# Kernel optimization log

Measured on AMD Instinct MI355X. Metric: run time of the kernel, lower is better.

Reference implementation:

```python
import jax, jax.numpy as jnp
import numpy as np

N, E, D, DE, DIN, L = 50000, 500000, 128, 16, 64, 4
EPS = 1e-5


def setup_inputs() -> dict:
    key = jax.random.key(0)
    ks = jax.random.split(key, 32)
    inp = {
        "x": jax.random.normal(ks[0], (N, DIN), dtype=jnp.float32),
        "edge_index": jax.random.randint(ks[1], (2, E), 0, N, dtype=jnp.int32),
        "edge_attr": jax.random.normal(ks[2], (E, DE), dtype=jnp.float32),
        "Win": jax.random.normal(ks[3], (DIN, D), dtype=jnp.float32) * 0.05,
        "b_in": jnp.zeros((D,), dtype=jnp.float32),
    }
    i = 4
    def lin(shape):
        nonlocal i
        w = jax.random.normal(ks[i], shape, dtype=jnp.float32) * 0.05
        i += 1
        return w
    def bn_params():
        nonlocal i
        g = jnp.ones((L, D), dtype=jnp.float32)
        b = jnp.zeros((L, D), dtype=jnp.float32)
        m = jax.random.normal(ks[i], (L, D), dtype=jnp.float32) * 0.1
        v = jax.random.uniform(ks[i + 1], (L, D), dtype=jnp.float32, minval=0.5, maxval=1.5)
        i += 2
        return g, b, m, v
    # message MLP: Linear(2D+DE -> D), BN, ReLU, Drop(eval), Linear(D -> D), BN, ReLU
    inp["Wm1"] = lin((L, 2 * D + DE, D)); inp["bm1"] = jnp.zeros((L, D), jnp.float32)
    inp["gm1"], inp["bem1"], inp["mm1"], inp["vm1"] = bn_params()
    inp["Wm2"] = lin((L, D, D)); inp["bm2"] = jnp.zeros((L, D), jnp.float32)
    inp["gm2"], inp["bem2"], inp["mm2"], inp["vm2"] = bn_params()
    # update MLP: Linear(2D -> D), BN, ReLU, Drop(eval), Linear(D -> D), BN, ReLU
    inp["Wu1"] = lin((L, 2 * D, D)); inp["bu1"] = jnp.zeros((L, D), jnp.float32)
    inp["gu1"], inp["beu1"], inp["mu1"], inp["vu1"] = bn_params()
    inp["Wu2"] = lin((L, D, D)); inp["bu2"] = jnp.zeros((L, D), jnp.float32)
    inp["gu2"], inp["beu2"], inp["mu2"], inp["vu2"] = bn_params()
    return inp


def _bn(x, g, b, m, v):
    # BatchNorm1d in eval mode: normalize with running stats
    return (x - m) * jax.lax.rsqrt(v + EPS) * g + b


def reference(x, edge_index, edge_attr, Win, b_in,
              Wm1, bm1, gm1, bem1, mm1, vm1,
              Wm2, bm2, gm2, bem2, mm2, vm2,
              Wu1, bu1, gu1, beu1, mu1, vu1,
              Wu2, bu2, gu2, beu2, mu2, vu2):
    h = x @ Win + b_in                       # (n, d)
    src, dst = edge_index[0], edge_index[1]  # PyG: row0 = source j, row1 = target i
    n = h.shape[0]
    num_layers = Wm1.shape[0]
    for l in range(num_layers):
        # message: concat(h_i, h_j, edge_attr) -> MLP psi
        m = jnp.concatenate([h[dst], h[src], edge_attr], axis=-1)   # (e, 2d+de)
        m = jax.nn.relu(_bn(m @ Wm1[l] + bm1[l], gm1[l], bem1[l], mm1[l], vm1[l]))
        m = jax.nn.relu(_bn(m @ Wm2[l] + bm2[l], gm2[l], bem2[l], mm2[l], vm2[l]))
        # aggregate: scatter-add messages to target nodes
        agg = jax.ops.segment_sum(m, dst, num_segments=n)           # (n, d)
        # update: concat(h, agg) -> MLP phi
        u = jnp.concatenate([h, agg], axis=-1)                      # (n, 2d)
        u = jax.nn.relu(_bn(u @ Wu1[l] + bu1[l], gu1[l], beu1[l], mu1[l], vu1[l]))
        u = jax.nn.relu(_bn(u @ Wu2[l] + bu2[l], gu2[l], beu2[l], mu2[l], vu2[l]))
        h = h + u                                                   # residual
    return h
```

## Files before the change

kernel.cpp:

```cpp
#include <hip/hip_runtime.h>
#include <hip/hip_fp16.h>

#define D 128
#define DE 16
#define NL 4
#define EPSV 1e-5f
#define S_U1 8
#define S_U2 4
#define NBMSG 512
#define MSG_LDS 75776

using f32x4  = __attribute__((ext_vector_type(4))) float;
using bf16x8 = __attribute__((ext_vector_type(8))) short;
typedef _Float16 f16x8 __attribute__((ext_vector_type(8)));

#define MFMAB(a, b, c) __builtin_amdgcn_mfma_f32_16x16x32_bf16((a), (b), (c), 0, 0, 0)
#define MFMAH(a, b, c) __builtin_amdgcn_mfma_f32_16x16x32_f16((a), (b), (c), 0, 0, 0)

union H8 { int4 i; unsigned int u[4]; f16x8 f; };

__device__ __forceinline__ unsigned short f2bf(float x) {
  unsigned int u = __float_as_uint(x);
  u = (u + 0x7FFFu + ((u >> 16) & 1u)) >> 16;
  return (unsigned short)u;
}

__device__ __forceinline__ unsigned short f2h(float x) {
  return __half_as_ushort(__float2half(x));
}

__device__ __forceinline__ float h2f(unsigned short x) {
  return __half2float(__ushort_as_half(x));
}

__device__ __forceinline__ unsigned int pk_add(unsigned int a, unsigned int b) {
  unsigned int r;
  asm("v_pk_add_f16 %0, %1, %2" : "=v"(r) : "v"(a), "v"(b));
  return r;
}
__device__ __forceinline__ unsigned int pk_relu(unsigned int a) {
  unsigned int r;
  asm("v_pk_max_f16 %0, %1, 0" : "=v"(r) : "v"(a));
  return r;
}

__device__ __forceinline__ void gload_lds16(const void* gp, void* lp) {
  typedef __attribute__((address_space(1))) unsigned int as1_u32;
  typedef __attribute__((address_space(3))) unsigned int as3_u32;
  __builtin_amdgcn_global_load_lds((as1_u32*)(unsigned long long)gp,
                                   (as3_u32*)(unsigned int)(unsigned long long)lp,
                                   16, 0, 0);
}

__device__ __forceinline__ bf16x8 pack8(float4 a, float4 b) {
  bf16x8 o;
  o[0] = (short)f2bf(a.x); o[1] = (short)f2bf(a.y);
  o[2] = (short)f2bf(a.z); o[3] = (short)f2bf(a.w);
  o[4] = (short)f2bf(b.x); o[5] = (short)f2bf(b.y);
  o[6] = (short)f2bf(b.z); o[7] = (short)f2bf(b.w);
  return o;
}

__device__ __forceinline__ int4 pack8h(float4 a, float4 b) {
  int4 o;
  o.x = (int)((unsigned)f2h(a.x) | ((unsigned)f2h(a.y) << 16));
  o.y = (int)((unsigned)f2h(a.z) | ((unsigned)f2h(a.w) << 16));
  o.z = (int)((unsigned)f2h(b.x) | ((unsigned)f2h(b.y) << 16));
  o.w = (int)((unsigned)f2h(b.z) | ((unsigned)f2h(b.w) << 16));
  return o;
}

__global__ void wprep_kernel(const float* __restrict__ W, const float* __restrict__ g,
                             const float* __restrict__ v, unsigned short* __restrict__ out,
                             int K, int S, int total) {
  int idx = blockIdx.x * 256 + threadIdx.x;
  if (idx >= total) return;
  int e = idx & 7, l0 = (idx >> 3) & 63, f = idx >> 9;
  int n = f & 7, sf = f >> 3, s = sf % S, l = sf / S;
  int k = s * 32 + ((l0 >> 4) << 3) + e;
  int c = (n << 4) + (l0 & 15);
  float val = 0.f;
  if (k < K) {
    float sc = g[l * D + c] * rsqrtf(v[l * D + c] + EPSV);
    val = W[((size_t)(l * K + k)) * D + c] * sc;
  }
  out[idx] = f2bf(val);
}

__global__ void wprep16_kernel(const float* __restrict__ W, const float* __restrict__ g,
                               const float* __restrict__ v, unsigned short* __restrict__ out,
                               int Ktot, int ko, int Kact, int S, int total) {
  int idx = blockIdx.x * 256 + threadIdx.x;
  if (idx >= total) return;
  int e = idx & 7, l0 = (idx >> 3) & 63, f = idx >> 9;
  int n = f & 7, sf = f >> 3, s = sf % S, l = sf / S;
  int k = s * 32 + ((l0 >> 4) << 3) + e;
  int c = (n << 4) + (l0 & 15);
  float val = 0.f;
  if (k < Kact) {
    float sc = g[l * D + c] * rsqrtf(v[l * D + c] + EPSV);
    val = W[((size_t)(l * Ktot + ko + k)) * D + c] * sc;
  }
  out[idx] = f2h(val);
}

__global__ void wprepz_kernel(const float* __restrict__ W1, const float* __restrict__ g,
                              const float* __restrict__ v, unsigned short* __restrict__ out,
                              int total) {
  int idx = blockIdx.x * 256 + threadIdx.x;
  if (idx >= total) return;
  int e = idx & 7, l0 = (idx >> 3) & 63, f = idx >> 9;
  int n = f & 15, sf = f >> 4, s = sf & 3, l = sf >> 2;
  int k = s * 32 + ((l0 >> 4) << 3) + e;
  int c = ((n & 7) << 4) + (l0 & 15);
  int row = (n < 8) ? k : 128 + k;
  float sc = g[l * D + c] * rsqrtf(v[l * D + c] + EPSV);
  float val = W1[((size_t)(l * 272 + row)) * D + c] * sc;
  out[idx] = f2bf(val);
}

__global__ void wprepx_kernel(const float* __restrict__ Win, unsigned short* __restrict__ out) {
  int idx = blockIdx.x * 256 + threadIdx.x;
  if (idx >= 8192) return;
  int e = idx & 7, l0 = (idx >> 3) & 63, f = idx >> 9;
  int n = f & 7, s = f >> 3;
  int k = s * 32 + ((l0 >> 4) << 3) + e;
  int c = (n << 4) + (l0 & 15);
  out[idx] = f2bf(Win[k * D + c]);
}

__global__ void cvtx_kernel(const float* __restrict__ x, unsigned short* __restrict__ xbf, int n8) {
  int idx = blockIdx.x * 256 + threadIdx.x;
  if (idx >= n8) return;
  float4 a = reinterpret_cast<const float4*>(x)[idx * 2];
  float4 b = reinterpret_cast<const float4*>(x)[idx * 2 + 1];
  reinterpret_cast<bf16x8*>(xbf)[idx] = pack8(a, b);
}

__global__ void bprep_kernel(const float* __restrict__ b, const float* __restrict__ g,
                             const float* __restrict__ be, const float* __restrict__ m,
                             const float* __restrict__ v, float* __restrict__ out) {
  int idx = blockIdx.x * 256 + threadIdx.x;
  if (idx >= NL * D) return;
  float s = g[idx] * rsqrtf(v[idx] + EPSV);
  out[idx] = (b[idx] - m[idx]) * s + be[idx];
}

__global__ __launch_bounds__(256)
void xz_kernel(const unsigned short* __restrict__ xbf,
               const unsigned short* __restrict__ Wxf,
               const float* __restrict__ bin,
               const unsigned short* __restrict__ Wzf,
               const float* __restrict__ b1,
               float* __restrict__ h,
               unsigned short* __restrict__ hbf,
               unsigned short* __restrict__ zds, int N) {
  __shared__ unsigned short m1ls[4][16 * 128];
  const int tid = threadIdx.x, wid = tid >> 6, lane = tid & 63, g = lane >> 4, r = lane & 15;
  const int nbase = blockIdx.x * 64;
  const int nr = nbase + wid * 16 + r;
  const int ar = (nr < N) ? nr : (N - 1);

  bf16x8 aX[2];
#pragma unroll
  for (int s = 0; s < 2; ++s)
    aX[s] = *reinterpret_cast<const bf16x8*>(xbf + (size_t)ar * 64 + s * 32 + g * 8);

  f32x4 acc[8];
#pragma unroll
  for (int n = 0; n < 8; ++n)
#pragma unroll
    for (int q = 0; q < 4; ++q) acc[n][q] = 0.f;
#pragma unroll
  for (int s = 0; s < 2; ++s)
#pragma unroll
    for (int n = 0; n < 8; ++n)
      acc[n] = MFMAB(aX[s], *reinterpret_cast<const bf16x8*>(Wxf + (((s * 8 + n) << 9) + (lane << 3))), acc[n]);

  float bia[8];
#pragma unroll
  for (int n = 0; n < 8; ++n) bia[n] = bin[n * 16 + r];

  unsigned short* m1w = &m1ls[wid][0];
#pragma unroll
  for (int j = 0; j < 4; ++j) {
    int node = nbase + wid * 16 + g * 4 + j;
    if (node < N) {
#pragma unroll
      for (int n = 0; n < 8; ++n) {
        int col = n * 16 + r;
        float hv = acc[n][j] + bia[n];
        h[(size_t)node * D + col] = hv;
        unsigned short hb = f2bf(hv);
        hbf[(size_t)node * D + col] = hb;
        int row0 = g * 4 + j;
        m1w[row0 * 128 + (col ^ ((row0 & 7) << 3))] = hb;
      }
    }
  }

  bf16x8 aZ[4];
#pragma unroll
  for (int s = 0; s < 4; ++s) {
    int k0 = s * 32 + g * 8;
    aZ[s] = *reinterpret_cast<const bf16x8*>(m1w + r * 128 + (k0 ^ ((r & 7) << 3)));
  }
  float bz[8];
#pragma unroll
  for (int n = 0; n < 8; ++n) bz[n] = b1[n * 16 + r];
#pragma unroll
  for (int half = 0; half < 2; ++half) {
    f32x4 zacc[8];
#pragma unroll
    for (int n = 0; n < 8; ++n)
#pragma unroll
      for (int q = 0; q < 4; ++q) zacc[n][q] = 0.f;
#pragma unroll
    for (int s = 0; s < 4; ++s)
#pragma unroll
      for (int n = 0; n < 8; ++n)
        zacc[n] = MFMAB(aZ[s], *reinterpret_cast<const bf16x8*>(Wzf + (((s * 16 + half * 8 + n) << 9) + (lane << 3))), zacc[n]);
#pragma unroll
    for (int n = 0; n < 8; ++n)
#pragma unroll
      for (int j = 0; j < 4; ++j) {
        int node = nbase + wid * 16 + g * 4 + j;
        if (node < N) {
          float v = zacc[n][j] + (half == 0 ? bz[n] : 0.f);
          zds[(size_t)node * 256 + (half * 8 + n) * 16 + r] = f2h(v);
        }
      }
  }
}

__global__ void hist_kernel(const int* __restrict__ eidx, int* __restrict__ hist, int E) {
  int e = blockIdx.x * 256 + threadIdx.x;
  if (e < E) atomicAdd(&hist[eidx[E + e]], 1);
}

__global__ void scan1_kernel(const int* __restrict__ hist, int* __restrict__ bsum, int N) {
  __shared__ int sb[256];
  int i = blockIdx.x * 256 + threadIdx.x;
  sb[threadIdx.x] = (i < N) ? hist[i] : 0;
  __syncthreads();
  for (int d = 128; d > 0; d >>= 1) {
    if (threadIdx.x < d) sb[threadIdx.x] += sb[threadIdx.x + d];
    __syncthreads();
  }
  if (threadIdx.x == 0) bsum[blockIdx.x] = sb[0];
}

__global__ void scan2_kernel(int* __restrict__ bsum, int nb) {
  __shared__ int sb[2][256];
  int t = threadIdx.x;
  int v = (t < nb) ? bsum[t] : 0;
  int p = 0;
  sb[0][t] = v; __syncthreads();
#pragma unroll
  for (int d = 1; d < 256; d <<= 1) {
    int nv = sb[p][t] + ((t >= d) ? sb[p][t - d] : 0);
    sb[p ^ 1][t] = nv; p ^= 1;
    __syncthreads();
  }
  if (t < nb) bsum[t] = sb[p][t] - v;
}

__global__ void scan3_kernel(int* __restrict__ hist, const int* __restrict__ bsum, int N) {
  __shared__ int sb[2][256];
  int i = blockIdx.x * 256 + threadIdx.x, t = threadIdx.x;
  int v = (i < N) ? hist[i] : 0;
  int p = 0;
  sb[0][t] = v; __syncthreads();
#pragma unroll
  for (int d = 1; d < 256; d <<= 1) {
    int nv = sb[p][t] + ((t >= d) ? sb[p][t - d] : 0);
    sb[p ^ 1][t] = nv; p ^= 1;
    __syncthreads();
  }
  if (i < N) hist[i] = sb[p][t] - v + bsum[blockIdx.x];
}

__global__ void scatter_kernel(const int* __restrict__ eidx, int* __restrict__ cursor,
                               int* __restrict__ dstS, int* __restrict__ srcS,
                               int* __restrict__ eidS, int E) {
  int e = blockIdx.x * 256 + threadIdx.x;
  if (e >= E) return;
  int d = eidx[E + e];
  int pos = atomicAdd(&cursor[d], 1);
  dstS[pos] = d;
  srcS[pos] = eidx[e];
  eidS[pos] = e;
}

__global__ void eperm_kernel(const float* __restrict__ eattr, const int* __restrict__ eidS,
                             unsigned short* __restrict__ ebfS, int E) {
  int i = blockIdx.x * 256 + threadIdx.x;
  if (i >= E) return;
  const float4* src = reinterpret_cast<const float4*>(eattr + (size_t)eidS[i] * DE);
  *reinterpret_cast<int4*>(ebfS + (size_t)i * DE) = pack8h(src[0], src[1]);
  *reinterpret_cast<int4*>(ebfS + (size_t)i * DE + 8) = pack8h(src[2], src[3]);
}

__global__ __launch_bounds__(512, 4)
void msg_kernel(const unsigned short* __restrict__ zds,
                const unsigned short* __restrict__ ebfS,
                const int* __restrict__ dstS,
                const int* __restrict__ srcS,
                const unsigned short* __restrict__ Wef,
                const unsigned short* __restrict__ W2f,
                const float* __restrict__ b2,
                unsigned short* __restrict__ msgb, int E, int T) {
  extern __shared__ char smem[];
  unsigned short* Wels = (unsigned short*)smem;
  unsigned short* W2ls = (unsigned short*)(smem + 8192);
  const int tid = threadIdx.x;
  const int wid = tid >> 6, lane = tid & 63, g = lane >> 4, r = lane & 15;
  unsigned short* zeb = (unsigned short*)(smem + 40960 + wid * 4352);

  gload_lds16(Wef + ((size_t)tid << 3), smem + (tid << 4));
#pragma unroll
  for (int i = 0; i < 4; ++i) {
    int idx = i * 512 + tid;
    gload_lds16(W2f + ((size_t)idx << 3), smem + 8192 + (idx << 4));
  }

  float bia2[8];
#pragma unroll
  for (int n = 0; n < 8; ++n) bia2[n] = b2[n * 16 + r];

  const int t0 = (int)(((long long)blockIdx.x * T) / gridDim.x);
  const int t1 = (int)(((long long)(blockIdx.x + 1) * T) / gridDim.x);

  __syncthreads();

  for (int t = t0; t < t1; ++t) {
    const int p0 = t * 128 + wid * 16 + r;
    const int ii0 = min(p0, E - 1);
    const int dst0 = dstS[ii0], src0 = srcS[ii0];

    H8 zd[4], zs[4];
#pragma unroll
    for (int s = 0; s < 4; ++s) {
      zd[s].i = *reinterpret_cast<const int4*>(zds + (size_t)dst0 * 256 + s * 32 + g * 8);
      zs[s].i = *reinterpret_cast<const int4*>(zds + (size_t)src0 * 256 + 128 + s * 32 + g * 8);
    }

    H8 aE;
    aE.i = make_int4(0, 0, 0, 0);
    if (g < 2) aE.i = *reinterpret_cast<const int4*>(ebfS + (size_t)ii0 * DE + g * 8);
    f32x4 ze[8];
#pragma unroll
    for (int n = 0; n < 8; ++n)
#pragma unroll
      for (int q = 0; q < 4; ++q) ze[n][q] = 0.f;
#pragma unroll
    for (int n = 0; n < 8; ++n) {
      f16x8 b = *reinterpret_cast<const f16x8*>(Wels + (n << 9) + (lane << 3));
      ze[n] = MFMAH(aE.f, b, ze[n]);
    }

#pragma unroll
    for (int n = 0; n < 8; ++n)
#pragma unroll
      for (int j = 0; j < 4; ++j) {
        int row = g * 4 + j;
        zeb[row * 136 + ((n * 2 + (r >> 3)) << 3) + (r & 7)] = f2h(ze[n][j]);
      }

    f32x4 c[8];
#pragma unroll
    for (int n = 0; n < 8; ++n)
#pragma unroll
      for (int q = 0; q < 4; ++q) c[n][q] = 0.f;

#pragma unroll
    for (int s = 0; s < 4; ++s) {
      H8 zeA, m;
      zeA.i = *reinterpret_cast<const int4*>(zeb + r * 136 + ((s * 4 + g) << 3));
#pragma unroll
      for (int w = 0; w < 4; ++w)
        m.u[w] = pk_relu(pk_add(pk_add(zd[s].u[w], zs[s].u[w]), zeA.u[w]));
      __builtin_amdgcn_s_setprio(1);
#pragma unroll
      for (int n = 0; n < 8; ++n) {
        f16x8 b = *reinterpret_cast<const f16x8*>(W2ls + ((s * 8 + n) << 9) + (lane << 3));
        c[n] = MFMAH(m.f, b, c[n]);
      }
      __builtin_amdgcn_s_setprio(0);
    }

#pragma unroll
    for (int n = 0; n < 8; ++n) {
      unsigned int lo = (unsigned)f2h(fmaxf(c[n][0] + bia2[n], 0.f))
                      | ((unsigned)f2h(fmaxf(c[n][1] + bia2[n], 0.f)) << 16);
      unsigned int hi = (unsigned)f2h(fmaxf(c[n][2] + bia2[n], 0.f))
                      | ((unsigned)f2h(fmaxf(c[n][3] + bia2[n], 0.f)) << 16);
      size_t addr8 = ((((size_t)t * 32 + wid * 4 + g) * 8 + n) * 16) + r;
      uint2 pk; pk.x = lo; pk.y = hi;
      *reinterpret_cast<uint2*>(msgb + addr8 * 4) = pk;
    }
  }
}

__global__ __launch_bounds__(256)
void reduce_kernel(const unsigned short* __restrict__ msgb,
                   const int* __restrict__ csr_end,
                   unsigned short* __restrict__ aggbf, int N) {
  const int tid = threadIdx.x, wid = tid >> 6, lane = tid & 63;
  const int er = lane >> 4, cg = lane & 15;
  for (int v = blockIdx.x * 4 + wid; v < N; v += gridDim.x * 4) {
    const int s = (v == 0) ? 0 : csr_end[v - 1];
    const int e = csr_end[v];
    float a[8];
#pragma unroll
    for (int n = 0; n < 8; ++n) a[n] = 0.f;
    const int qe = (e + 3) >> 2;
    for (int qb = (s >> 2); qb < qe; qb += 4) {
      int q = qb + er;
      if (q < qe) {
        size_t base8 = (size_t)q * 128 + cg;
        int p0 = 4 * q;
#pragma unroll
        for (int n = 0; n < 8; ++n) {
          uint2 d = *reinterpret_cast<const uint2*>(msgb + (base8 + (size_t)n * 16) * 4);
          float v0 = h2f((unsigned short)(d.x & 0xffff));
          float v1 = h2f((unsigned short)(d.x >> 16));
          float v2 = h2f((unsigned short)(d.y & 0xffff));
          float v3 = h2f((unsigned short)(d.y >> 16));
          a[n] += ((p0 >= s && p0 < e) ? v0 : 0.f)
                + ((p0 + 1 >= s && p0 + 1 < e) ? v1 : 0.f)
                + ((p0 + 2 >= s && p0 + 2 < e) ? v2 : 0.f)
                + ((p0 + 3 >= s && p0 + 3 < e) ? v3 : 0.f);
        }
      }
    }
#pragma unroll
    for (int n = 0; n < 8; ++n) {
      a[n] += __shfl_xor(a[n], 16);
      a[n] += __shfl_xor(a[n], 32);
    }
    if (er == 0) {
#pragma unroll
      for (int n = 0; n < 8; ++n)
        aggbf[(size_t)v * 128 + n * 16 + cg] = f2bf(a[n]);
    }
  }
}

__global__ __launch_bounds__(256, 3)
void node_kernel(const unsigned short* __restrict__ hbf,
                 const unsigned short* __restrict__ aggbf,
                 const unsigned short* __restrict__ W1f,
                 const unsigned short* __restrict__ W2f,
                 const float* __restrict__ b1,
                 const float* __restrict__ b2,
                 float* __restrict__ h,
                 unsigned short* __restrict__ hbfo,
                 const unsigned short* __restrict__ Wzf,
                 const float* __restrict__ b1n,
                 unsigned short* __restrict__ zds, int N) {
  __shared__ unsigned short m1ls[4][16 * 128];

  const int tid = threadIdx.x, wid = tid >> 6, lane = tid & 63, g = lane >> 4, r = lane & 15;
  const int nbase = blockIdx.x * 64;
  const int nr0 = nbase + wid * 16 + r;
  const int ar0 = (nr0 < N) ? nr0 : (N - 1);

  bf16x8 aH0[4], aG0[4];
#pragma unroll
  for (int s = 0; s < 4; ++s) {
    aH0[s] = *reinterpret_cast<const bf16x8*>(hbf + (size_t)ar0 * D + s * 32 + g * 8);
    aG0[s] = *reinterpret_cast<const bf16x8*>(aggbf + (size_t)ar0 * D + s * 32 + g * 8);
  }

  float hv[4][8];
#pragma unroll
  for (int j = 0; j < 4; ++j) {
    int node = nbase + wid * 16 + g * 4 + j;
    int an = (node < N) ? node : (N - 1);
#pragma unroll
    for (int n = 0; n < 8; ++n)
      hv[j][n] = h[(size_t)an * D + n * 16 + r];
  }

  float bia1[8], bia2[8];
#pragma unroll
  for (int n = 0; n < 8; ++n) { bia1[n] = b1[n * 16 + r]; bia2[n] = b2[n * 16 + r]; }

  f32x4 acc0[8];
#pragma unroll
  for (int n = 0; n < 8; ++n)
#pragma unroll
    for (int q = 0; q < 4; ++q) acc0[n][q] = 0.f;

#pragma unroll
  for (int s = 0; s < S_U1; ++s) {
    bf16x8 a0 = (s < 4) ? aH0[s & 3] : aG0[(s - 4) & 3];
#pragma unroll
    for (int n = 0; n < 8; ++n) {
      bf16x8 b = *reinterpret_cast<const bf16x8*>(W1f + (((s * 8 + n) << 9) + (lane << 3)));
      acc0[n] = MFMAB(a0, b, acc0[n]);
    }
  }

  unsigned short* m1w = &m1ls[wid][0];
#pragma unroll
  for (int n = 0; n < 8; ++n)
#pragma unroll
    for (int j = 0; j < 4; ++j) {
      int col = n * 16 + r;
      int row0 = g * 4 + j;
      m1w[row0 * 128 + (col ^ ((row0 & 7) << 3))] = f2bf(fmaxf(acc0[n][j] + bia1[n], 0.f));
    }

  f32x4 c0[8];
#pragma unroll
  for (int n = 0; n < 8; ++n)
#pragma unroll
    for (int q = 0; q < 4; ++q) c0[n][q] = 0.f;

#pragma unroll
  for (int s = 0; s < S_U2; ++s) {
    int k0 = s * 32 + g * 8;
    bf16x8 a0 = *reinterpret_cast<const bf16x8*>(m1w + r * 128 + (k0 ^ ((r & 7) << 3)));
#pragma unroll
    for (int n = 0; n < 8; ++n) {
      bf16x8 b = *reinterpret_cast<const bf16x8*>(W2f + (((s * 8 + n) << 9) + (lane << 3)));
      c0[n] = MFMAB(a0, b, c0[n]);
    }
  }

#pragma unroll
  for (int j = 0; j < 4; ++j) {
    int node = nbase + wid * 16 + g * 4 + j;
    if (node < N) {
#pragma unroll
      for (int n = 0; n < 8; ++n) {
        int col = n * 16 + r;
        float hvnew = hv[j][n] + fmaxf(c0[n][j] + bia2[n], 0.f);
        h[(size_t)node * D + col] = hvnew;
        unsigned short hb = f2bf(hvnew);
        hbfo[(size_t)node * D + col] = hb;
        int row0 = g * 4 + j;
        m1w[row0 * 128 + (col ^ ((row0 & 7) << 3))] = hb;
      }
    }
  }

  if (Wzf != nullptr) {
    bf16x8 aZ[4];
#pragma unroll
    for (int s = 0; s < 4; ++s) {
      int k0 = s * 32 + g * 8;
      aZ[s] = *reinterpret_cast<const bf16x8*>(m1w + r * 128 + (k0 ^ ((r & 7) << 3)));
    }
    float bz[8];
#pragma unroll
    for (int n = 0; n < 8; ++n) bz[n] = b1n[n * 16 + r];
#pragma unroll
    for (int half = 0; half < 2; ++half) {
      f32x4 zacc[8];
#pragma unroll
      for (int n = 0; n < 8; ++n)
#pragma unroll
        for (int q = 0; q < 4; ++q) zacc[n][q] = 0.f;
#pragma unroll
      for (int s = 0; s < 4; ++s)
#pragma unroll
        for (int n = 0; n < 8; ++n)
          zacc[n] = MFMAB(aZ[s], *reinterpret_cast<const bf16x8*>(Wzf + (((s * 16 + half * 8 + n) << 9) + (lane << 3))), zacc[n]);
#pragma unroll
      for (int n = 0; n < 8; ++n)
#pragma unroll
        for (int j = 0; j < 4; ++j) {
          int node = nbase + wid * 16 + g * 4 + j;
          if (node < N) {
            float v = zacc[n][j] + (half == 0 ? bz[n] : 0.f);
            zds[(size_t)node * 256 + (half * 8 + n) * 16 + r] = f2h(v);
          }
        }
    }
  }
}

extern "C" void kernel_launch(void* const* d_in, const int* in_sizes, int n_in,
                              void* d_out, int out_size, void* d_ws, size_t ws_size,
                              hipStream_t stream) {
  const float* x     = (const float*)d_in[0];
  const int*   eidx  = (const int*)d_in[1];
  const float* eattr = (const float*)d_in[2];
  const float* Win   = (const float*)d_in[3];
  const float* bin   = (const float*)d_in[4];
  const float* Wm1 = (const float*)d_in[5];  const float* bm1 = (const float*)d_in[6];
  const float* gm1 = (const float*)d_in[7];  const float* bem1 = (const float*)d_in[8];
  const float* mm1 = (const float*)d_in[9];  const float* vm1 = (const float*)d_in[10];
  const float* Wm2 = (const float*)d_in[11]; const float* bm2 = (const float*)d_in[12];
  const float* gm2 = (const float*)d_in[13]; const float* bem2 = (const float*)d_in[14];
  const float* mm2 = (const float*)d_in[15]; const float* vm2 = (const float*)d_in[16];
  const float* Wu1 = (const float*)d_in[17]; const float* bu1 = (const float*)d_in[18];
  const float* gu1 = (const float*)d_in[19]; const float* beu1 = (const float*)d_in[20];
  const float* mu1 = (const float*)d_in[21]; const float* vu1 = (const float*)d_in[22];
  const float* Wu2 = (const float*)d_in[23]; const float* bu2 = (const float*)d_in[24];
  const float* gu2 = (const float*)d_in[25]; const float* beu2 = (const float*)d_in[26];
  const float* mu2 = (const float*)d_in[27]; const float* vu2 = (const float*)d_in[28];

  const int N = in_sizes[0] / 64;
  const int E = in_sizes[1] / 2;
  float* h = (float*)d_out;

  const int T = (E + 127) / 128;
  const size_t Epad = (size_t)T * 128;

  char* ws = (char*)d_ws;
  size_t off = 0;
  unsigned short* aggbf = (unsigned short*)(ws + off); off += (size_t)N * D * 2;
  unsigned short* hbf   = (unsigned short*)(ws + off); off += (size_t)N * D * 2;
  unsigned short* zds   = (unsigned short*)(ws + off); off += (size_t)N * 256 * 2;
  unsigned short* xbf   = (unsigned short*)(ws + off); off += (size_t)N * 64 * 2;
  unsigned short* ebfS  = (unsigned short*)(ws + off); off += (size_t)E * DE * 2;
  int* dstS = (int*)(ws + off);                        off += (size_t)E * 4;
  int* srcS = (int*)(ws + off);                        off += (size_t)E * 4;
  int* eidS = (int*)(ws + off);                        off += (size_t)E * 4;
  int* hist = (int*)(ws + off);                        off += ((size_t)N * 4 + 15) & ~15ull;
  int* bsum = (int*)(ws + off);                        off += 1024;
  unsigned short* Wef   = (unsigned short*)(ws + off); off += (size_t)NL * 4096 * 2;
  unsigned short* W2f16 = (unsigned short*)(ws + off); off += (size_t)NL * 16384 * 2;
  unsigned short* Wzf   = (unsigned short*)(ws + off); off += (size_t)NL * 32768 * 2;
  unsigned short* Wu1f  = (unsigned short*)(ws + off); off += (size_t)NL * S_U1 * 4096 * 2;
  unsigned short* Wu2f  = (unsigned short*)(ws + off); off += (size_t)NL * S_U2 * 4096 * 2;
  unsigned short* Wxf   = (unsigned short*)(ws + off); off += (size_t)8192 * 2;
  float* bm1f = (float*)(ws + off); off += (size_t)NL * D * 4;
  float* bm2f = (float*)(ws + off); off += (size_t)NL * D * 4;
  float* bu1f = (float*)(ws + off); off += (size_t)NL * D * 4;
  float* bu2f = (float*)(ws + off); off += (size_t)NL * D * 4;
  unsigned short* msgb = (unsigned short*)(ws + off);  off += Epad * 128 * 2;
  if (off > ws_size) return;

  (void)hipFuncSetAttribute(reinterpret_cast<const void*>(msg_kernel),
                            hipFuncAttributeMaxDynamicSharedMemorySize, MSG_LDS);

  {
    int tWe = NL * 4096, tW2 = NL * 16384, tWz = NL * 32768;
    int tU1 = NL * S_U1 * 4096, tU2 = NL * S_U2 * 4096;
    wprep16_kernel<<<(tWe + 255) / 256, 256, 0, stream>>>(Wm1, gm1, vm1, Wef, 272, 256, 16, 1, tWe);
    wprep16_kernel<<<(tW2 + 255) / 256, 256, 0, stream>>>(Wm2, gm2, vm2, W2f16, 128, 0, 128, 4, tW2);
    wprepz_kernel<<<(tWz + 255) / 256, 256, 0, stream>>>(Wm1, gm1, vm1, Wzf, tWz);
    wprep_kernel<<<(tU1 + 255) / 256, 256, 0, stream>>>(Wu1, gu1, vu1, Wu1f, 2 * D, S_U1, tU1);
    wprep_kernel<<<(tU2 + 255) / 256, 256, 0, stream>>>(Wu2, gu2, vu2, Wu2f, D, S_U2, tU2);
    wprepx_kernel<<<32, 256, 0, stream>>>(Win, Wxf);
    cvtx_kernel<<<(N * 8 + 255) / 256, 256, 0, stream>>>(x, xbf, N * 8);
    bprep_kernel<<<2, 256, 0, stream>>>(bm1, gm1, bem1, mm1, vm1, bm1f);
    bprep_kernel<<<2, 256, 0, stream>>>(bm2, gm2, bem2, mm2, vm2, bm2f);
    bprep_kernel<<<2, 256, 0, stream>>>(bu1, gu1, beu1, mu1, vu1, bu1f);
    bprep_kernel<<<2, 256, 0, stream>>>(bu2, gu2, beu2, mu2, vu2, bu2f);
  }

  {
    const int NB_H = (N + 255) / 256;
    (void)hipMemsetAsync(hist, 0, (size_t)N * 4, stream);
    hist_kernel<<<(E + 255) / 256, 256, 0, stream>>>(eidx, hist, E);
    scan1_kernel<<<NB_H, 256, 0, stream>>>(hist, bsum, N);
    scan2_kernel<<<1, 256, 0, stream>>>(bsum, NB_H);
    scan3_kernel<<<NB_H, 256, 0, stream>>>(hist, bsum, N);
    scatter_kernel<<<(E + 255) / 256, 256, 0, stream>>>(eidx, hist, dstS, srcS, eidS, E);
    eperm_kernel<<<(E + 255) / 256, 256, 0, stream>>>(eattr, eidS, ebfS, E);
  }

  const int nblocks = (N + 63) / 64;
  xz_kernel<<<nblocks, 256, 0, stream>>>(xbf, Wxf, bin, Wzf, bm1f, h, hbf, zds, N);

  for (int l = 0; l < NL; ++l) {
    msg_kernel<<<NBMSG, 512, MSG_LDS, stream>>>(zds, ebfS, dstS, srcS,
                                                Wef + (size_t)l * 4096,
                                                W2f16 + (size_t)l * 16384,
                                                bm2f + l * D, msgb, E, T);
    reduce_kernel<<<2048, 256, 0, stream>>>(msgb, hist, aggbf, N);
    const unsigned short* WzNext = (l < NL - 1) ? (Wzf + (size_t)(l + 1) * 32768) : nullptr;
    const float* b1Next = bm1f + ((l < NL - 1) ? (l + 1) : 0) * D;
    node_kernel<<<nblocks, 256, 0, stream>>>(hbf, aggbf,
                                             Wu1f + (size_t)l * S_U1 * 4096,
                                             Wu2f + (size_t)l * S_U2 * 4096,
                                             bu1f + l * D, bu2f + l * D, h, hbf,
                                             WzNext, b1Next, zds, N);
  }
}
```

Before: 599.2 us.

## Fuse message aggregation into msg kernel via fp32 atomics on sorted destinations

The message kernel now accumulates messages directly into an fp32 aggregate buffer with atomic adds. It run-length merges consecutive edges that share a destination, which works because edges are sorted by destination. This replaces the fp16 message buffer write and the separate CSR reduce kernel. It adds a per-layer memset and an fp32-to-bf16 conversion kernel, and raises node_kernel's occupancy hint from 3 to 6 blocks. The trade-off is that memory traffic is removed at the cost of atomic contention and non-deterministic summation order.

Result: slower. 1.110 ms (+85.2%).

```diff
diff --git a/kernel.cpp b/kernel.cpp
--- a/kernel.cpp
+++ b/kernel.cpp
@@ -27,10 +27,6 @@
 
 __device__ __forceinline__ unsigned short f2h(float x) {
   return __half_as_ushort(__float2half(x));
-}
-
-__device__ __forceinline__ float h2f(unsigned short x) {
-  return __half2float(__ushort_as_half(x));
 }
 
 __device__ __forceinline__ unsigned int pk_add(unsigned int a, unsigned int b) {
@@ -144,6 +140,14 @@
   if (idx >= NL * D) return;
   float s = g[idx] * rsqrtf(v[idx] + EPSV);
   out[idx] = (b[idx] - m[idx]) * s + be[idx];
+}
+
+__global__ void agg2bf_kernel(const float* __restrict__ agg, unsigned short* __restrict__ aggbf, int n8) {
+  int idx = blockIdx.x * 256 + threadIdx.x;
+  if (idx >= n8) return;
+  float4 a = reinterpret_cast<const float4*>(agg)[idx * 2];
+  float4 b = reinterpret_cast<const float4*>(agg)[idx * 2 + 1];
+  reinterpret_cast<bf16x8*>(aggbf)[idx] = pack8(a, b);
 }
 
 __global__ __launch_bounds__(256)
@@ -309,7 +313,7 @@
                 const unsigned short* __restrict__ Wef,
                 const unsigned short* __restrict__ W2f,
                 const float* __restrict__ b2,
-                unsigned short* __restrict__ msgb, int E, int T) {
+                float* __restrict__ agg, int E, int T) {
   extern __shared__ char smem[];
   unsigned short* Wels = (unsigned short*)smem;
   unsigned short* W2ls = (unsigned short*)(smem + 8192);
@@ -389,65 +393,30 @@
       __builtin_amdgcn_s_setprio(0);
     }
 
+    int dm[4];
+#pragma unroll
+    for (int j = 0; j < 4; ++j) dm[j] = __shfl(dst0, g * 4 + j, 64);
 #pragma unroll
     for (int n = 0; n < 8; ++n) {
-      unsigned int lo = (unsigned)f2h(fmaxf(c[n][0] + bia2[n], 0.f))
-                      | ((unsigned)f2h(fmaxf(c[n][1] + bia2[n], 0.f)) << 16);
-      unsigned int hi = (unsigned)f2h(fmaxf(c[n][2] + bia2[n], 0.f))
-                      | ((unsigned)f2h(fmaxf(c[n][3] + bia2[n], 0.f)) << 16);
-      size_t addr8 = ((((size_t)t * 32 + wid * 4 + g) * 8 + n) * 16) + r;
-      uint2 pk; pk.x = lo; pk.y = hi;
-      *reinterpret_cast<uint2*>(msgb + addr8 * 4) = pk;
-    }
-  }
-}
-
-__global__ __launch_bounds__(256)
-void reduce_kernel(const unsigned short* __restrict__ msgb,
-                   const int* __restrict__ csr_end,
-                   unsigned short* __restrict__ aggbf, int N) {
-  const int tid = threadIdx.x, wid = tid >> 6, lane = tid & 63;
-  const int er = lane >> 4, cg = lane & 15;
-  for (int v = blockIdx.x * 4 + wid; v < N; v += gridDim.x * 4) {
-    const int s = (v == 0) ? 0 : csr_end[v - 1];
-    const int e = csr_end[v];
-    float a[8];
-#pragma unroll
-    for (int n = 0; n < 8; ++n) a[n] = 0.f;
-    const int qe = (e + 3) >> 2;
-    for (int qb = (s >> 2); qb < qe; qb += 4) {
-      int q = qb + er;
-      if (q < qe) {
-        size_t base8 = (size_t)q * 128 + cg;
-        int p0 = 4 * q;
-#pragma unroll
-        for (int n = 0; n < 8; ++n) {
-          uint2 d = *reinterpret_cast<const uint2*>(msgb + (base8 + (size_t)n * 16) * 4);
-          float v0 = h2f((unsigned short)(d.x & 0xffff));
-          float v1 = h2f((unsigned short)(d.x >> 16));
-          float v2 = h2f((unsigned short)(d.y & 0xffff));
-          float v3 = h2f((unsigned short)(d.y >> 16));
-          a[n] += ((p0 >= s && p0 < e) ? v0 : 0.f)
-                + ((p0 + 1 >= s && p0 + 1 < e) ? v1 : 0.f)
-                + ((p0 + 2 >= s && p0 + 2 < e) ? v2 : 0.f)
-                + ((p0 + 3 >= s && p0 + 3 < e) ? v3 : 0.f);
+      float run = 0.f; int dcur = -1;
+#pragma unroll
+      for (int j = 0; j < 4; ++j) {
+        int eg = t * 128 + wid * 16 + g * 4 + j;
+        float vv = fmaxf(c[n][j] + bia2[n], 0.f);
+        if (eg < E) {
+          if (dm[j] != dcur) {
+            if (dcur >= 0) unsafeAtomicAdd(agg + (size_t)dcur * D + n * 16 + r, run);
+            dcur = dm[j]; run = 0.f;
+          }
+          run += vv;
         }
       }
-    }
-#pragma unroll
-    for (int n = 0; n < 8; ++n) {
-      a[n] += __shfl_xor(a[n], 16);
-      a[n] += __shfl_xor(a[n], 32);
-    }
-    if (er == 0) {
-#pragma unroll
-      for (int n = 0; n < 8; ++n)
-        aggbf[(size_t)v * 128 + n * 16 + cg] = f2bf(a[n]);
-    }
-  }
-}
-
-__global__ __launch_bounds__(256, 3)
+      if (dcur >= 0) unsafeAtomicAdd(agg + (size_t)dcur * D + n * 16 + r, run);
+    }
+  }
+}
+
+__global__ __launch_bounds__(256, 6)
 void node_kernel(const unsigned short* __restrict__ hbf,
                  const unsigned short* __restrict__ aggbf,
                  const unsigned short* __restrict__ W1f,
@@ -609,10 +578,10 @@
   float* h = (float*)d_out;
 
   const int T = (E + 127) / 128;
-  const size_t Epad = (size_t)T * 128;
 
   char* ws = (char*)d_ws;
   size_t off = 0;
+  float* agg = (float*)(ws + off);                     off += (size_t)N * D * 4;
   unsigned short* aggbf = (unsigned short*)(ws + off); off += (size_t)N * D * 2;
   unsigned short* hbf   = (unsigned short*)(ws + off); off += (size_t)N * D * 2;
   unsigned short* zds   = (unsigned short*)(ws + off); off += (size_t)N * 256 * 2;
@@ -633,7 +602,6 @@
   float* bm2f = (float*)(ws + off); off += (size_t)NL * D * 4;
   float* bu1f = (float*)(ws + off); off += (size_t)NL * D * 4;
   float* bu2f = (float*)(ws + off); off += (size_t)NL * D * 4;
-  unsigned short* msgb = (unsigned short*)(ws + off);  off += Epad * 128 * 2;
   if (off > ws_size) return;
 
   (void)hipFuncSetAttribute(reinterpret_cast<const void*>(msg_kernel),
@@ -669,12 +637,14 @@
   const int nblocks = (N + 63) / 64;
   xz_kernel<<<nblocks, 256, 0, stream>>>(xbf, Wxf, bin, Wzf, bm1f, h, hbf, zds, N);
 
+  const int n8 = N * D / 8;
   for (int l = 0; l < NL; ++l) {
+    (void)hipMemsetAsync(agg, 0, (size_t)N * D * 4, stream);
     msg_kernel<<<NBMSG, 512, MSG_LDS, stream>>>(zds, ebfS, dstS, srcS,
                                                 Wef + (size_t)l * 4096,
                                                 W2f16 + (size_t)l * 16384,
-                                                bm2f + l * D, msgb, E, T);
-    reduce_kernel<<<2048, 256, 0, stream>>>(msgb, hist, aggbf, N);
+                                                bm2f + l * D, agg, E, T);
+    agg2bf_kernel<<<(n8 + 255) / 256, 256, 0, stream>>>(agg, aggbf, n8);
     const unsigned short* WzNext = (l < NL - 1) ? (Wzf + (size_t)(l + 1) * 32768) : nullptr;
     const float* b1Next = bm1f + ((l < NL - 1) ? (l + 1) : 0) * D;
     node_kernel<<<nblocks, 256, 0, stream>>>(hbf, aggbf,
```
